# Kernel optimization log

Measured on AMD Instinct MI355X. Metric: run time of the kernel, lower is better.

Reference implementation:

```python
import jax, jax.numpy as jnp
from jax import lax
import numpy as np

H = 48; W = 48; C_IN = 256; A_PER = 3
M = A_PER * H * W            # 6912 anchors
IMG = 768.0                  # square image, clip bound for x and y
OBJ_THR = 0.3; IOU_THR = 0.7; TOP_K = 2000
NEG = -1e9                   # finite sentinel for masked scores


def _make_anchors():
    stride = IMG / H
    base = 2.0 * stride
    ratios = np.array([0.5, 1.0, 2.0])
    ws = base * np.sqrt(ratios)          # [3]
    hs = base / np.sqrt(ratios)
    cx = (np.arange(W) + 0.5) * stride
    cy = (np.arange(H) + 0.5) * stride
    cxg, cyg = np.meshgrid(cx, cy)       # [H, W]
    anc = np.stack([
        cxg[None] - ws[:, None, None] / 2,
        cyg[None] - hs[:, None, None] / 2,
        cxg[None] + ws[:, None, None] / 2,
        cyg[None] + hs[:, None, None] / 2,
    ], axis=-1)                           # [3, H, W, 4] matches (anchor, h, w) flatten order
    return jnp.asarray(anc.reshape(-1, 4), jnp.float32)


def setup_inputs() -> dict:
    key = jax.random.key(0)
    ks = jax.random.split(key, 4)
    x = jax.random.normal(ks[0], (1, C_IN, H, W), jnp.float32)
    conv_w = jax.random.normal(ks[1], (256, 256, 3, 3), jnp.float32) * 0.02
    conv_b = jnp.zeros((256,), jnp.float32)
    det_w = jax.random.normal(ks[2], (3, 256, 1, 1), jnp.float32) * 0.02
    det_b = jnp.zeros((3,), jnp.float32)
    reg_w = jax.random.normal(ks[3], (12, 256, 1, 1), jnp.float32) * 0.02
    reg_b = jnp.zeros((12,), jnp.float32)
    anchors = _make_anchors()
    return {"x": x, "conv_w": conv_w, "conv_b": conv_b, "det_w": det_w,
            "det_b": det_b, "reg_w": reg_w, "reg_b": reg_b, "anchors": anchors}


def reference(x, conv_w, conv_b, det_w, det_b, reg_w, reg_b, anchors):
    # ---- FPN 3x3 conv + RPN head (1x1 convs) ----
    inter = lax.conv_general_dilated(
        x, conv_w, (1, 1), 'SAME',
        dimension_numbers=('NCHW', 'OIHW', 'NCHW')) + conv_b[None, :, None, None]
    obj = jax.nn.sigmoid(jnp.einsum('nchw,oc->nohw', inter, det_w[:, :, 0, 0])
                         + det_b[None, :, None, None])          # [1,3,H,W]
    reg = (jnp.einsum('nchw,oc->nohw', inter, reg_w[:, :, 0, 0])
           + reg_b[None, :, None, None])                        # [1,12,H,W]

    scores = obj.reshape(-1)                                    # [M], (anchor,h,w) order
    deltas = reg.reshape(1, 4, A_PER, H, W).transpose(0, 2, 3, 4, 1).reshape(-1, 4)

    # ---- box decode (preserves the source's cx/cy quirk: cx = y1 + w/2, cy = x1 + h/2) ----
    x1, y1, x2, y2 = anchors[:, 0], anchors[:, 1], anchors[:, 2], anchors[:, 3]
    aw = x2 - x1; ah = y2 - y1
    acx = y1 + aw / 2; acy = x1 + ah / 2
    dx, dy, dw, dh = deltas[:, 0], deltas[:, 1], deltas[:, 2], deltas[:, 3]
    px = acx + dx * aw; py = acy + dy * ah
    pw = aw * jnp.exp(dw); ph = ah * jnp.exp(dh)
    boxes = jnp.stack([px - pw / 2, py - ph / 2, px + pw / 2, py + ph / 2], axis=-1)

    # ---- clip to image ----
    boxes = jnp.clip(boxes, 0.0, IMG)

    # ---- validity: degenerate filter (source's naming quirk) + objectness threshold ----
    hts = boxes[:, 2] - boxes[:, 0]
    wds = boxes[:, 3] - boxes[:, 1]
    valid = (hts > 0) & (wds > 0) & (scores > OBJ_THR)

    # ---- greedy NMS (jit-friendly: sort, pairwise IoU, sequential suppression) ----
    s = jnp.where(valid, scores, NEG)
    order = jnp.argsort(-s)
    b = boxes[order]; v = valid[order]; ss = s[order]
    area = (b[:, 2] - b[:, 0]) * (b[:, 3] - b[:, 1])             # [M]
    iw = jnp.clip(jnp.minimum(b[:, None, 2], b[None, :, 2])
                  - jnp.maximum(b[:, None, 0], b[None, :, 0]), 0.0)
    ih = jnp.clip(jnp.minimum(b[:, None, 3], b[None, :, 3])
                  - jnp.maximum(b[:, None, 1], b[None, :, 1]), 0.0)
    inter_a = iw * ih                                             # [M,M]
    iou = inter_a / jnp.maximum(area[:, None] + area[None, :] - inter_a, 1e-9)

    idx = jnp.arange(M)

    def body(suppressed, i):
        keep_i = v[i] & (~suppressed[i])
        sup = keep_i & (iou[i] > IOU_THR) & (idx > i)
        return suppressed | sup, keep_i

    _, keeps = lax.scan(body, jnp.zeros(M, bool), idx)            # keep mask (sorted order)

    # ---- top-k proposal selection (fixed K, padded with sentinels) ----
    out_s = jnp.where(keeps, ss, NEG)
    topv, topi = lax.top_k(out_s, TOP_K)
    vtop = keeps[topi]
    out_scores = jnp.where(vtop, topv, -1.0)                      # [TOP_K]
    out_boxes = jnp.where(vtop[:, None], b[topi], 0.0)            # [TOP_K, 4]
    return out_scores, out_boxes
```

## Files before the change

kernel.cpp:

```cpp
#include <hip/hip_runtime.h>
#include <cstdint>

#define NPX 2304
#define MM 6912
#define NW 108
#define TOPK 2000
#define NEGV -1000000000.0f
#define OBJ_THRF 0.3f
#define IOU_THRF 0.7f
#define IMGF 768.0f
#define KSPLIT 8

typedef unsigned long long u64;
typedef unsigned int u32;

__device__ __forceinline__ u64 shfl64(u64 v, int src) {
  int lo = __shfl((int)(v & 0xffffffffull), src, 64);
  int hi = __shfl((int)(v >> 32), src, 64);
  return ((u64)(u32)hi << 32) | (u32)lo;
}

__global__ __launch_bounds__(256) void k_wt(const float* __restrict__ cw,
                                            float* __restrict__ wt) {
  __shared__ float t[64][65];
  const int it0 = blockIdx.x * 64;
  const int oc0 = blockIdx.y * 64;
  const int tx = threadIdx.x & 63;
  const int ty = threadIdx.x >> 6;
#pragma unroll
  for (int k = 0; k < 16; ++k) {
    int oc = ty + k * 4;
    t[oc][tx] = cw[(oc0 + oc) * 2304 + it0 + tx];
  }
  __syncthreads();
#pragma unroll
  for (int k = 0; k < 16; ++k) {
    int it = ty + k * 4;
    wt[(it0 + it) * 256 + oc0 + tx] = t[tx][it];
  }
}

__global__ __launch_bounds__(256) void k_conv(const float* __restrict__ x,
                                              const float* __restrict__ wt,
                                              float* __restrict__ part) {
  __shared__ float xs[16 * 8 * 52];
  const int tid = threadIdx.x;
  const int px = blockIdx.x * 256 + tid;
  const int oc0 = blockIdx.y * 16;
  const int ks = blockIdx.z;
  const int row = px / 48, col = px % 48;
  const int r0 = (blockIdx.x * 256) / 48;
  const int rbase = row - r0;

  float acc[16];
#pragma unroll
  for (int k = 0; k < 16; ++k) acc[k] = 0.f;

  for (int icc = 0; icc < 2; ++icc) {
    const int ic0 = ks * 32 + icc * 16;
    for (int e = tid; e < 16 * 8 * 50; e += 256) {
      int ic = e / 400, rem = e % 400;
      int r = rem / 50, c = rem % 50 - 1;
      int gr = r0 - 1 + r;
      float v = 0.f;
      if (c >= 0 && c < 48 && gr >= 0 && gr < 48)
        v = x[(ic0 + ic) * NPX + gr * 48 + c];
      xs[(ic * 8 + r) * 52 + (c + 1)] = v;
    }
    __syncthreads();
    for (int ic = 0; ic < 16; ++ic) {
      float xv[9];
#pragma unroll
      for (int dr = 0; dr < 3; ++dr)
#pragma unroll
        for (int dc = 0; dc < 3; ++dc)
          xv[dr * 3 + dc] = xs[(ic * 8 + rbase + dr) * 52 + col + dc];
      const float* wrow = wt + (size_t)(ic0 + ic) * 9 * 256 + oc0;
#pragma unroll
      for (int t = 0; t < 9; ++t) {
        const float* wp = wrow + t * 256;
#pragma unroll
        for (int k = 0; k < 16; ++k) acc[k] += xv[t] * wp[k];
      }
    }
    __syncthreads();
  }
#pragma unroll
  for (int k = 0; k < 16; ++k)
    part[((size_t)ks * 256 + oc0 + k) * NPX + px] = acc[k];
}

__global__ __launch_bounds__(256) void k_decode(const float* __restrict__ part,
                                                const float* __restrict__ cb,
                                                const float* __restrict__ dw,
                                                const float* __restrict__ db,
                                                const float* __restrict__ rw,
                                                const float* __restrict__ rb,
                                                const float* __restrict__ anch,
                                                float* __restrict__ s,
                                                float4* __restrict__ boxes) {
  __shared__ float wl[256 * 16];
  __shared__ float red[4 * 64 * 17];
  const int tid = threadIdx.x;
  const int pxl = tid & 63;
  const int cq = tid >> 6;
  const int px = blockIdx.x * 64 + pxl;
  for (int e = tid; e < 3840; e += 256) {
    int o = e % 15, c = e / 15;
    wl[c * 16 + o] = (o < 3) ? dw[o * 256 + c] : rw[(o - 3) * 256 + c];
  }
  __syncthreads();
  float acc[15];
#pragma unroll
  for (int o = 0; o < 15; o++) acc[o] = 0.f;
  for (int ci = 0; ci < 64; ++ci) {
    int c = cq * 64 + ci;
    float v = cb[c];
#pragma unroll
    for (int kks = 0; kks < KSPLIT; ++kks)
      v += part[((size_t)kks * 256 + c) * NPX + px];
#pragma unroll
    for (int o = 0; o < 15; o++) acc[o] += v * wl[c * 16 + o];
  }
#pragma unroll
  for (int o = 0; o < 15; o++) red[(cq * 64 + pxl) * 17 + o] = acc[o];
  __syncthreads();
  if (tid < 64) {
    const int p = blockIdx.x * 64 + tid;
    float a[15];
#pragma unroll
    for (int o = 0; o < 15; o++)
      a[o] = red[tid * 17 + o] + red[(64 + tid) * 17 + o] +
             red[(128 + tid) * 17 + o] + red[(192 + tid) * 17 + o];
    const float4* an4 = (const float4*)anch;
#pragma unroll
    for (int aa = 0; aa < 3; ++aa) {
      int m = aa * NPX + p;
      float logit = a[aa] + db[aa];
      float score = 1.f / (1.f + expf(-logit));
      float dxv = a[3 + 0 + aa] + rb[0 + aa];
      float dyv = a[3 + 3 + aa] + rb[3 + aa];
      float dwv = a[3 + 6 + aa] + rb[6 + aa];
      float dhv = a[3 + 9 + aa] + rb[9 + aa];
      float4 an = an4[m];
      float aw = an.z - an.x;
      float ah = an.w - an.y;
      float acx = an.y + aw * 0.5f;
      float acy = an.x + ah * 0.5f;
      float pxc = acx + dxv * aw;
      float pyc = acy + dyv * ah;
      float pw = aw * expf(dwv);
      float ph = ah * expf(dhv);
      float b0 = pxc - pw * 0.5f, b1 = pyc - ph * 0.5f;
      float b2 = pxc + pw * 0.5f, b3 = pyc + ph * 0.5f;
      b0 = fminf(fmaxf(b0, 0.f), IMGF);
      b1 = fminf(fmaxf(b1, 0.f), IMGF);
      b2 = fminf(fmaxf(b2, 0.f), IMGF);
      b3 = fminf(fmaxf(b3, 0.f), IMGF);
      float hts = b2 - b0, wds = b3 - b1;
      bool valid = (hts > 0.f) && (wds > 0.f) && (score > OBJ_THRF);
      s[m] = valid ? score : NEGV;
      boxes[m] = make_float4(b0, b1, b2, b3);
    }
  }
}

__global__ __launch_bounds__(256) void k_sortA(const float* __restrict__ s,
                                               u64* __restrict__ keys) {
  __shared__ u64 lds[1024];
  const int tid = threadIdx.x;
  const int b = blockIdx.x;
  for (int v = tid; v < 1024; v += 256) {
    int i = b * 1024 + v;
    u64 p;
    if (i < MM) {
      u32 u = __float_as_uint(s[i]);
      u = u ^ (u32)(((int)u >> 31) | 0x80000000);
      p = ((u64)(~u) << 32) | (u32)i;
    } else {
      p = ~0ull;
    }
    lds[v] = p;
  }
  for (u32 kk = 2; kk <= 1024; kk <<= 1) {
    for (u32 j = kk >> 1; j > 0; j >>= 1) {
      __syncthreads();
#pragma unroll 2
      for (int t = tid; t < 512; t += 256) {
        int i = ((t & ~(j - 1)) << 1) | (t & (j - 1));
        int l = i | j;
        bool up = ((i & kk) == 0);
        u64 a = lds[i], c = lds[l];
        u64 mn = a < c ? a : c;
        u64 mx = a < c ? c : a;
        lds[i] = up ? mn : mx;
        lds[l] = up ? mx : mn;
      }
    }
  }
  __syncthreads();
  for (int v = tid; v < 1024; v += 256) keys[b * 1024 + v] = lds[v];
}

__global__ __launch_bounds__(256) void k_merge(const u64* __restrict__ in,
                                               u64* __restrict__ outk, int L, int fin,
                                               const float* __restrict__ s,
                                               const float4* __restrict__ boxes,
                                               float* __restrict__ ssc,
                                               float4* __restrict__ sboxes) {
  const int i = blockIdx.x * 256 + threadIdx.x;
  const int pair = i / (2 * L);
  const int r = i - pair * 2 * L;
  const u64* A = in + (size_t)pair * 2 * L;
  const u64* B = A + L;
  int lo = (r > L) ? (r - L) : 0;
  int hi = (r < L) ? r : L;
  while (lo < hi) {
    int mid = (lo + hi) >> 1;
    if (A[mid] < B[r - 1 - mid]) lo = mid + 1; else hi = mid;
  }
  int a = lo, bi = r - lo;
  u64 av = (a < L) ? A[a] : ~0ull;
  u64 bv = (bi < L) ? B[bi] : ~0ull;
  u64 o = (av < bv) ? av : bv;
  outk[i] = o;
  if (fin && i < MM) {
    int idx = (int)(u32)o;
    ssc[i] = s[idx];
    sboxes[i] = boxes[idx];
  }
}

__global__ __launch_bounds__(256) void k_zero(u64* __restrict__ nz) {
  int i = blockIdx.x * 256 + threadIdx.x;
  if (i < MM * 2) nz[i] = 0;
}

__global__ __launch_bounds__(256) void k_mask(const float4* __restrict__ sboxes,
                                              u64* __restrict__ mask_t,
                                              u64* __restrict__ nz) {
  __shared__ float4 rb_[64];
  const int rt = blockIdx.x;
  const int w = blockIdx.y * 4 + (threadIdx.x >> 6);
  const int lane = threadIdx.x & 63;
  if (threadIdx.x < 64) rb_[threadIdx.x] = sboxes[rt * 64 + threadIdx.x];
  __syncthreads();
  if (w < rt) return;
  float4 c = sboxes[w * 64 + lane];
  float areaC = (c.z - c.x) * (c.w - c.y);
  u64 myw = 0;
  for (int r = 0; r < 64; ++r) {
    float4 b = rb_[r];
    float iw = fmaxf(fminf(b.z, c.z) - fmaxf(b.x, c.x), 0.f);
    float ih = fmaxf(fminf(b.w, c.w) - fmaxf(b.y, c.y), 0.f);
    float inter = iw * ih;
    float areaB = (b.z - b.x) * (b.w - b.y);
    float un = fmaxf(areaB + areaC - inter, 1e-9f);
    bool bit = (inter / un) > IOU_THRF;
    u64 bal = __ballot(bit);
    if (lane == r) myw = bal;
  }
  mask_t[(size_t)w * MM + rt * 64 + lane] = myw;
  if (myw) atomicOr(&nz[(rt * 64 + lane) * 2 + (w >> 6)], 1ull << (w & 63));
}

__global__ __launch_bounds__(256) void k_scan(const u64* __restrict__ mask_t,
                                              const u64* __restrict__ nz,
                                              const float* __restrict__ ssc,
                                              const float4* __restrict__ sboxes,
                                              float* __restrict__ out) {
  __shared__ u64 remv[NW];
  __shared__ u64 keepw[NW];
  __shared__ int blist[64];
  __shared__ int nkS;
  __shared__ int kcntS;
  __shared__ int pref[NW];
  const int tid = threadIdx.x;
  if (tid < NW) { remv[tid] = 0; keepw[tid] = 0; }
  if (tid == 0) kcntS = 0;
  __syncthreads();

  for (int c = 0; c < NW; ++c) {
    if (tid < 64) {
      const int lane = tid;
      u64 dg = mask_t[(size_t)c * MM + c * 64 + lane];
      float sv = ssc[c * 64 + lane];
      u64 vb = __ballot(sv > OBJ_THRF);
      u64 w0 = remv[c];
      u64 cand = vb & ~w0;
      u64 above = (lane < 63) ? ~((2ull << lane) - 1ull) : 0ull;
      bool inC = ((cand >> lane) & 1ull) != 0;
      u64 conf = __ballot(inC && ((dg & above & cand) != 0ull));
      u64 kb;
      if (conf == 0ull) {
        kb = cand;
      } else {
        u64 w = w0;
        kb = 0;
        u64 rem = cand;
        while (rem) {
          int b = __ffsll(rem) - 1;
          kb |= (1ull << b);
          w |= shfl64(dg, b);
          rem = vb & ~w;
        }
      }
      int below = __popcll(kb & ((1ull << lane) - 1ull));
      if ((kb >> lane) & 1ull) blist[below] = lane;
      if (lane == 0) {
        keepw[c] = kb;
        nkS = __popcll(kb);
        kcntS += __popcll(kb);
      }
    }
    __syncthreads();
    int nk = nkS;
    if (tid < nk) {
      int row = c * 64 + blist[tid];
      u64 nz0 = nz[row * 2], nz1 = nz[row * 2 + 1];
      if (c < 64) {
        nz0 &= (c < 63) ? ~((2ull << c) - 1ull) : 0ull;
      } else {
        nz0 = 0;
        int cc = c - 64;
        nz1 &= ~((2ull << cc) - 1ull);
      }
      while (nz0) {
        int wv = __ffsll(nz0) - 1; nz0 &= nz0 - 1;
        atomicOr(&remv[wv], mask_t[(size_t)wv * MM + row]);
      }
      while (nz1) {
        int wv = __ffsll(nz1) - 1; nz1 &= nz1 - 1;
        atomicOr(&remv[wv + 64], mask_t[(size_t)(wv + 64) * MM + row]);
      }
    }
    __syncthreads();
    if (kcntS >= TOPK) break;
  }

  if (tid == 0) {
    int run = 0;
    for (int cc = 0; cc < NW; ++cc) { pref[cc] = run; run += __popcll(keepw[cc]); }
  }
  __syncthreads();
  for (int e = tid; e < TOPK * 5; e += 256) out[e] = (e < TOPK) ? -1.0f : 0.0f;
  __syncthreads();
  float4* ob = (float4*)(out + TOPK);
  for (int i = tid; i < MM; i += 256) {
    int cc = i >> 6, b = i & 63;
    u64 kb = keepw[cc];
    if ((kb >> b) & 1ull) {
      int rank = pref[cc] + __popcll(kb & ((1ull << b) - 1ull));
      if (rank < TOPK) {
        out[rank] = ssc[i];
        ob[rank] = sboxes[i];
      }
    }
  }
}

extern "C" void kernel_launch(void* const* d_in, const int* in_sizes, int n_in,
                              void* d_out, int out_size, void* d_ws, size_t ws_size,
                              hipStream_t stream) {
  const float* x  = (const float*)d_in[0];
  const float* cw = (const float*)d_in[1];
  const float* cb = (const float*)d_in[2];
  const float* dw = (const float*)d_in[3];
  const float* db = (const float*)d_in[4];
  const float* rw = (const float*)d_in[5];
  const float* rb = (const float*)d_in[6];
  const float* an = (const float*)d_in[7];
  char* ws = (char*)d_ws;
  float*  part   = (float*)(ws);
  u64*    keysA  = (u64*)(ws);
  u64*    keysB  = (u64*)(ws + 65536);
  u64*    mask   = (u64*)(ws);
  u64*    nz     = (u64*)(ws + 5971968);
  float*  wt     = (float*)(ws + 18874368);
  float*  s      = (float*)(ws + 21233664);
  float4* boxes  = (float4*)(ws + 21261312);
  float*  ssc    = (float*)(ws + 21371904);
  float4* sboxes = (float4*)(ws + 21399552);
  float* out = (float*)d_out;

  hipLaunchKernelGGL(k_wt, dim3(36, 4), dim3(256), 0, stream, cw, wt);
  hipLaunchKernelGGL(k_conv, dim3(9, 16, KSPLIT), dim3(256), 0, stream, x, wt, part);
  hipLaunchKernelGGL(k_decode, dim3(36), dim3(256), 0, stream, part, cb, dw, db, rw, rb, an, s, boxes);
  hipLaunchKernelGGL(k_zero, dim3(54), dim3(256), 0, stream, nz);
  hipLaunchKernelGGL(k_sortA, dim3(8), dim3(256), 0, stream, s, keysA);
  hipLaunchKernelGGL(k_merge, dim3(32), dim3(256), 0, stream, keysA, keysB, 1024, 0, s, boxes, ssc, sboxes);
  hipLaunchKernelGGL(k_merge, dim3(32), dim3(256), 0, stream, keysB, keysA, 2048, 0, s, boxes, ssc, sboxes);
  hipLaunchKernelGGL(k_merge, dim3(32), dim3(256), 0, stream, keysA, keysB, 4096, 1, s, boxes, ssc, sboxes);
  hipLaunchKernelGGL(k_mask, dim3(108, 27), dim3(256), 0, stream, sboxes, mask, nz);
  hipLaunchKernelGGL(k_scan, dim3(1), dim3(256), 0, stream, mask, nz, ssc, sboxes, out);
}
```

Measured before the change: 267.2 us.

## Halve conv output-channel tile and split decode into parallel partial and finish kernels

The conv kernel now computes 8 output channels per block instead of 16, with smaller input-channel chunks, which doubles the grid to raise occupancy and parallelism. The decode stage is split into k_dq, which spreads the channel quarters across 144 small blocks and writes partial sums to workspace, and k_dfin, which reduces those sums and decodes boxes. This replaces the single 36-block decode that leaned on shared memory. The cost is one extra kernel launch, an extra global round trip for the partials, and more reloading of the halo input per conv block.

```diff
diff --git a/kernel.cpp b/kernel.cpp
--- a/kernel.cpp
+++ b/kernel.cpp
@@ -43,22 +43,22 @@
 __global__ __launch_bounds__(256) void k_conv(const float* __restrict__ x,
                                               const float* __restrict__ wt,
                                               float* __restrict__ part) {
-  __shared__ float xs[16 * 8 * 52];
+  __shared__ float xs[8 * 8 * 52];
   const int tid = threadIdx.x;
   const int px = blockIdx.x * 256 + tid;
-  const int oc0 = blockIdx.y * 16;
+  const int oc0 = blockIdx.y * 8;
   const int ks = blockIdx.z;
   const int row = px / 48, col = px % 48;
   const int r0 = (blockIdx.x * 256) / 48;
   const int rbase = row - r0;
 
-  float acc[16];
-#pragma unroll
-  for (int k = 0; k < 16; ++k) acc[k] = 0.f;
-
-  for (int icc = 0; icc < 2; ++icc) {
-    const int ic0 = ks * 32 + icc * 16;
-    for (int e = tid; e < 16 * 8 * 50; e += 256) {
+  float acc[8];
+#pragma unroll
+  for (int k = 0; k < 8; ++k) acc[k] = 0.f;
+
+  for (int icc = 0; icc < 4; ++icc) {
+    const int ic0 = ks * 32 + icc * 8;
+    for (int e = tid; e < 8 * 8 * 50; e += 256) {
       int ic = e / 400, rem = e % 400;
       int r = rem / 50, c = rem % 50 - 1;
       int gr = r0 - 1 + r;
@@ -68,7 +68,7 @@
       xs[(ic * 8 + r) * 52 + (c + 1)] = v;
     }
     __syncthreads();
-    for (int ic = 0; ic < 16; ++ic) {
+    for (int ic = 0; ic < 8; ++ic) {
       float xv[9];
 #pragma unroll
       for (int dr = 0; dr < 3; ++dr)
@@ -80,39 +80,35 @@
       for (int t = 0; t < 9; ++t) {
         const float* wp = wrow + t * 256;
 #pragma unroll
-        for (int k = 0; k < 16; ++k) acc[k] += xv[t] * wp[k];
+        for (int k = 0; k < 8; ++k) acc[k] += xv[t] * wp[k];
       }
     }
     __syncthreads();
   }
 #pragma unroll
-  for (int k = 0; k < 16; ++k)
+  for (int k = 0; k < 8; ++k)
     part[((size_t)ks * 256 + oc0 + k) * NPX + px] = acc[k];
 }
 
-__global__ __launch_bounds__(256) void k_decode(const float* __restrict__ part,
-                                                const float* __restrict__ cb,
-                                                const float* __restrict__ dw,
-                                                const float* __restrict__ db,
-                                                const float* __restrict__ rw,
-                                                const float* __restrict__ rb,
-                                                const float* __restrict__ anch,
-                                                float* __restrict__ s,
-                                                float4* __restrict__ boxes) {
-  __shared__ float wl[256 * 16];
-  __shared__ float red[4 * 64 * 17];
+__global__ __launch_bounds__(64) void k_dq(const float* __restrict__ part,
+                                           const float* __restrict__ cb,
+                                           const float* __restrict__ dw,
+                                           const float* __restrict__ rw,
+                                           float* __restrict__ qacc) {
+  __shared__ float wl[64 * 16];
   const int tid = threadIdx.x;
-  const int pxl = tid & 63;
-  const int cq = tid >> 6;
-  const int px = blockIdx.x * 64 + pxl;
-  for (int e = tid; e < 3840; e += 256) {
-    int o = e % 15, c = e / 15;
-    wl[c * 16 + o] = (o < 3) ? dw[o * 256 + c] : rw[(o - 3) * 256 + c];
+  const int cq = blockIdx.y;
+  const int px = blockIdx.x * 64 + tid;
+  for (int e = tid; e < 960; e += 64) {
+    int o = e % 15, ci = e / 15;
+    int c = cq * 64 + ci;
+    wl[ci * 16 + o] = (o < 3) ? dw[o * 256 + c] : rw[(o - 3) * 256 + c];
   }
   __syncthreads();
   float acc[15];
 #pragma unroll
   for (int o = 0; o < 15; o++) acc[o] = 0.f;
+#pragma unroll 4
   for (int ci = 0; ci < 64; ++ci) {
     int c = cq * 64 + ci;
     float v = cb[c];
@@ -120,48 +116,57 @@
     for (int kks = 0; kks < KSPLIT; ++kks)
       v += part[((size_t)kks * 256 + c) * NPX + px];
 #pragma unroll
-    for (int o = 0; o < 15; o++) acc[o] += v * wl[c * 16 + o];
-  }
-#pragma unroll
-  for (int o = 0; o < 15; o++) red[(cq * 64 + pxl) * 17 + o] = acc[o];
-  __syncthreads();
-  if (tid < 64) {
-    const int p = blockIdx.x * 64 + tid;
-    float a[15];
-#pragma unroll
-    for (int o = 0; o < 15; o++)
-      a[o] = red[tid * 17 + o] + red[(64 + tid) * 17 + o] +
-             red[(128 + tid) * 17 + o] + red[(192 + tid) * 17 + o];
-    const float4* an4 = (const float4*)anch;
-#pragma unroll
-    for (int aa = 0; aa < 3; ++aa) {
-      int m = aa * NPX + p;
-      float logit = a[aa] + db[aa];
-      float score = 1.f / (1.f + expf(-logit));
-      float dxv = a[3 + 0 + aa] + rb[0 + aa];
-      float dyv = a[3 + 3 + aa] + rb[3 + aa];
-      float dwv = a[3 + 6 + aa] + rb[6 + aa];
-      float dhv = a[3 + 9 + aa] + rb[9 + aa];
-      float4 an = an4[m];
-      float aw = an.z - an.x;
-      float ah = an.w - an.y;
-      float acx = an.y + aw * 0.5f;
-      float acy = an.x + ah * 0.5f;
-      float pxc = acx + dxv * aw;
-      float pyc = acy + dyv * ah;
-      float pw = aw * expf(dwv);
-      float ph = ah * expf(dhv);
-      float b0 = pxc - pw * 0.5f, b1 = pyc - ph * 0.5f;
-      float b2 = pxc + pw * 0.5f, b3 = pyc + ph * 0.5f;
-      b0 = fminf(fmaxf(b0, 0.f), IMGF);
-      b1 = fminf(fmaxf(b1, 0.f), IMGF);
-      b2 = fminf(fmaxf(b2, 0.f), IMGF);
-      b3 = fminf(fmaxf(b3, 0.f), IMGF);
-      float hts = b2 - b0, wds = b3 - b1;
-      bool valid = (hts > 0.f) && (wds > 0.f) && (score > OBJ_THRF);
-      s[m] = valid ? score : NEGV;
-      boxes[m] = make_float4(b0, b1, b2, b3);
-    }
+    for (int o = 0; o < 15; o++) acc[o] += v * wl[ci * 16 + o];
+  }
+#pragma unroll
+  for (int o = 0; o < 15; o++)
+    qacc[((size_t)cq * NPX + px) * 16 + o] = acc[o];
+}
+
+__global__ __launch_bounds__(64) void k_dfin(const float* __restrict__ qacc,
+                                             const float* __restrict__ db,
+                                             const float* __restrict__ rb,
+                                             const float* __restrict__ anch,
+                                             float* __restrict__ s,
+                                             float4* __restrict__ boxes) {
+  const int tid = threadIdx.x;
+  const int p = blockIdx.x * 64 + tid;
+  float a[15];
+#pragma unroll
+  for (int o = 0; o < 15; o++)
+    a[o] = qacc[((size_t)0 * NPX + p) * 16 + o] +
+           qacc[((size_t)1 * NPX + p) * 16 + o] +
+           qacc[((size_t)2 * NPX + p) * 16 + o] +
+           qacc[((size_t)3 * NPX + p) * 16 + o];
+  const float4* an4 = (const float4*)anch;
+#pragma unroll
+  for (int aa = 0; aa < 3; ++aa) {
+    int m = aa * NPX + p;
+    float logit = a[aa] + db[aa];
+    float score = 1.f / (1.f + expf(-logit));
+    float dxv = a[3 + 0 + aa] + rb[0 + aa];
+    float dyv = a[3 + 3 + aa] + rb[3 + aa];
+    float dwv = a[3 + 6 + aa] + rb[6 + aa];
+    float dhv = a[3 + 9 + aa] + rb[9 + aa];
+    float4 an = an4[m];
+    float aw = an.z - an.x;
+    float ah = an.w - an.y;
+    float acx = an.y + aw * 0.5f;
+    float acy = an.x + ah * 0.5f;
+    float pxc = acx + dxv * aw;
+    float pyc = acy + dyv * ah;
+    float pw = aw * expf(dwv);
+    float ph = ah * expf(dhv);
+    float b0 = pxc - pw * 0.5f, b1 = pyc - ph * 0.5f;
+    float b2 = pxc + pw * 0.5f, b3 = pyc + ph * 0.5f;
+    b0 = fminf(fmaxf(b0, 0.f), IMGF);
+    b1 = fminf(fmaxf(b1, 0.f), IMGF);
+    b2 = fminf(fmaxf(b2, 0.f), IMGF);
+    b3 = fminf(fmaxf(b3, 0.f), IMGF);
+    float hts = b2 - b0, wds = b3 - b1;
+    bool valid = (hts > 0.f) && (wds > 0.f) && (score > OBJ_THRF);
+    s[m] = valid ? score : NEGV;
+    boxes[m] = make_float4(b0, b1, b2, b3);
   }
 }
 
@@ -377,6 +382,7 @@
   u64*    mask   = (u64*)(ws);
   u64*    nz     = (u64*)(ws + 5971968);
   float*  wt     = (float*)(ws + 18874368);
+  float*  qacc   = (float*)(ws + 18874368);
   float*  s      = (float*)(ws + 21233664);
   float4* boxes  = (float4*)(ws + 21261312);
   float*  ssc    = (float*)(ws + 21371904);
@@ -384,8 +390,9 @@
   float* out = (float*)d_out;
 
   hipLaunchKernelGGL(k_wt, dim3(36, 4), dim3(256), 0, stream, cw, wt);
-  hipLaunchKernelGGL(k_conv, dim3(9, 16, KSPLIT), dim3(256), 0, stream, x, wt, part);
-  hipLaunchKernelGGL(k_decode, dim3(36), dim3(256), 0, stream, part, cb, dw, db, rw, rb, an, s, boxes);
+  hipLaunchKernelGGL(k_conv, dim3(9, 32, KSPLIT), dim3(256), 0, stream, x, wt, part);
+  hipLaunchKernelGGL(k_dq, dim3(36, 4), dim3(64), 0, stream, part, cb, dw, rw, qacc);
+  hipLaunchKernelGGL(k_dfin, dim3(36), dim3(64), 0, stream, qacc, db, rb, an, s, boxes);
   hipLaunchKernelGGL(k_zero, dim3(54), dim3(256), 0, stream, nz);
   hipLaunchKernelGGL(k_sortA, dim3(8), dim3(256), 0, stream, s, keysA);
   hipLaunchKernelGGL(k_merge, dim3(32), dim3(256), 0, stream, keysA, keysB, 1024, 0, s, boxes, ssc, sboxes);
```

Result: slower. 282.6 us (+5.8%).

## Fuse merge passes into one LDS kernel, fold nz zeroing, preload scan data

Applied to the files above, without the earlier changes.

Replaces three global-memory merge-pass launches with one 1024-thread block that runs all merge passes in shared memory, and folds the nz zeroing into the sort kernel, removing four launches. The serial scan kernel now preloads the diagonal mask words and sorted scores into LDS, so the per-chunk loop no longer waits on global loads. The cost is that the merges run on a single CU, and the scan kernel uses more shared memory (about 83 KB), which limits it to one block.

```diff
diff --git a/kernel.cpp b/kernel.cpp
--- a/kernel.cpp
+++ b/kernel.cpp
@@ -166,10 +166,12 @@
 }
 
 __global__ __launch_bounds__(256) void k_sortA(const float* __restrict__ s,
-                                               u64* __restrict__ keys) {
+                                               u64* __restrict__ keys,
+                                               u64* __restrict__ nz) {
   __shared__ u64 lds[1024];
   const int tid = threadIdx.x;
   const int b = blockIdx.x;
+  for (int i = b * 256 + tid; i < MM * 2; i += 8 * 256) nz[i] = 0;
   for (int v = tid; v < 1024; v += 256) {
     int i = b * 1024 + v;
     u64 p;
@@ -202,38 +204,45 @@
   for (int v = tid; v < 1024; v += 256) keys[b * 1024 + v] = lds[v];
 }
 
-__global__ __launch_bounds__(256) void k_merge(const u64* __restrict__ in,
-                                               u64* __restrict__ outk, int L, int fin,
-                                               const float* __restrict__ s,
-                                               const float4* __restrict__ boxes,
-                                               float* __restrict__ ssc,
-                                               float4* __restrict__ sboxes) {
-  const int i = blockIdx.x * 256 + threadIdx.x;
-  const int pair = i / (2 * L);
-  const int r = i - pair * 2 * L;
-  const u64* A = in + (size_t)pair * 2 * L;
-  const u64* B = A + L;
-  int lo = (r > L) ? (r - L) : 0;
-  int hi = (r < L) ? r : L;
-  while (lo < hi) {
-    int mid = (lo + hi) >> 1;
-    if (A[mid] < B[r - 1 - mid]) lo = mid + 1; else hi = mid;
-  }
-  int a = lo, bi = r - lo;
-  u64 av = (a < L) ? A[a] : ~0ull;
-  u64 bv = (bi < L) ? B[bi] : ~0ull;
-  u64 o = (av < bv) ? av : bv;
-  outk[i] = o;
-  if (fin && i < MM) {
-    int idx = (int)(u32)o;
+__global__ __launch_bounds__(1024) void k_mtail(const u64* __restrict__ keysA,
+                                                const float* __restrict__ s,
+                                                const float4* __restrict__ boxes,
+                                                float* __restrict__ ssc,
+                                                float4* __restrict__ sboxes) {
+  __shared__ u64 A[8192];
+  __shared__ u64 B[8192];
+  const int tid = threadIdx.x;
+  for (int v = tid; v < 8192; v += 1024) A[v] = keysA[v];
+  __syncthreads();
+
+  const u64* in = A;
+  u64* out = B;
+#pragma unroll 1
+  for (int L = 1024; L <= 4096; L <<= 1) {
+    for (int i = tid; i < 8192; i += 1024) {
+      int pair = i / (2 * L);
+      int r = i - pair * 2 * L;
+      const u64* Ap = in + pair * 2 * L;
+      const u64* Bp = Ap + L;
+      int lo = (r > L) ? (r - L) : 0;
+      int hi = (r < L) ? r : L;
+      while (lo < hi) {
+        int mid = (lo + hi) >> 1;
+        if (Ap[mid] < Bp[r - 1 - mid]) lo = mid + 1; else hi = mid;
+      }
+      int a = lo, bi = r - lo;
+      u64 av = (a < L) ? Ap[a] : ~0ull;
+      u64 bv = (bi < L) ? Bp[bi] : ~0ull;
+      out[i] = (av < bv) ? av : bv;
+    }
+    __syncthreads();
+    const u64* t = in; in = out; out = (u64*)t;
+  }
+  for (int i = tid; i < MM; i += 1024) {
+    int idx = (int)(u32)in[i];
     ssc[i] = s[idx];
     sboxes[i] = boxes[idx];
   }
-}
-
-__global__ __launch_bounds__(256) void k_zero(u64* __restrict__ nz) {
-  int i = blockIdx.x * 256 + threadIdx.x;
-  if (i < MM * 2) nz[i] = 0;
 }
 
 __global__ __launch_bounds__(256) void k_mask(const float4* __restrict__ sboxes,
@@ -269,6 +278,8 @@
                                               const float* __restrict__ ssc,
                                               const float4* __restrict__ sboxes,
                                               float* __restrict__ out) {
+  __shared__ u64 diagL[NW * 64];
+  __shared__ float sscL[MM];
   __shared__ u64 remv[NW];
   __shared__ u64 keepw[NW];
   __shared__ int blist[64];
@@ -276,6 +287,9 @@
   __shared__ int kcntS;
   __shared__ int pref[NW];
   const int tid = threadIdx.x;
+  for (int e = tid; e < NW * 64; e += 256)
+    diagL[e] = mask_t[(size_t)(e >> 6) * MM + (e >> 6) * 64 + (e & 63)];
+  for (int e = tid; e < MM; e += 256) sscL[e] = ssc[e];
   if (tid < NW) { remv[tid] = 0; keepw[tid] = 0; }
   if (tid == 0) kcntS = 0;
   __syncthreads();
@@ -283,8 +297,8 @@
   for (int c = 0; c < NW; ++c) {
     if (tid < 64) {
       const int lane = tid;
-      u64 dg = mask_t[(size_t)c * MM + c * 64 + lane];
-      float sv = ssc[c * 64 + lane];
+      u64 dg = diagL[c * 64 + lane];
+      float sv = sscL[c * 64 + lane];
       u64 vb = __ballot(sv > OBJ_THRF);
       u64 w0 = remv[c];
       u64 cand = vb & ~w0;
@@ -352,7 +366,7 @@
     if ((kb >> b) & 1ull) {
       int rank = pref[cc] + __popcll(kb & ((1ull << b) - 1ull));
       if (rank < TOPK) {
-        out[rank] = ssc[i];
+        out[rank] = sscL[i];
         ob[rank] = sboxes[i];
       }
     }
@@ -373,7 +387,6 @@
   char* ws = (char*)d_ws;
   float*  part   = (float*)(ws);
   u64*    keysA  = (u64*)(ws);
-  u64*    keysB  = (u64*)(ws + 65536);
   u64*    mask   = (u64*)(ws);
   u64*    nz     = (u64*)(ws + 5971968);
   float*  wt     = (float*)(ws + 18874368);
@@ -386,11 +399,8 @@
   hipLaunchKernelGGL(k_wt, dim3(36, 4), dim3(256), 0, stream, cw, wt);
   hipLaunchKernelGGL(k_conv, dim3(9, 16, KSPLIT), dim3(256), 0, stream, x, wt, part);
   hipLaunchKernelGGL(k_decode, dim3(36), dim3(256), 0, stream, part, cb, dw, db, rw, rb, an, s, boxes);
-  hipLaunchKernelGGL(k_zero, dim3(54), dim3(256), 0, stream, nz);
-  hipLaunchKernelGGL(k_sortA, dim3(8), dim3(256), 0, stream, s, keysA);
-  hipLaunchKernelGGL(k_merge, dim3(32), dim3(256), 0, stream, keysA, keysB, 1024, 0, s, boxes, ssc, sboxes);
-  hipLaunchKernelGGL(k_merge, dim3(32), dim3(256), 0, stream, keysB, keysA, 2048, 0, s, boxes, ssc, sboxes);
-  hipLaunchKernelGGL(k_merge, dim3(32), dim3(256), 0, stream, keysA, keysB, 4096, 1, s, boxes, ssc, sboxes);
+  hipLaunchKernelGGL(k_sortA, dim3(8), dim3(256), 0, stream, s, keysA, nz);
+  hipLaunchKernelGGL(k_mtail, dim3(1), dim3(1024), 0, stream, keysA, s, boxes, ssc, sboxes);
   hipLaunchKernelGGL(k_mask, dim3(108, 27), dim3(256), 0, stream, sboxes, mask, nz);
   hipLaunchKernelGGL(k_scan, dim3(1), dim3(256), 0, stream, mask, nz, ssc, sboxes, out);
 }
```

Result: slower. 292.8 us (+9.6%).

## Parallelize NMS suppression updates and stage diagonal masks in LDS

Applied to the files above, without the earlier changes.

The single-block NMS scan now preloads all diagonal mask words and sorted scores into shared memory, and prefetches each chunk's nonzero-word bitmap into LDS. The per-kept-box serial loop over suppression words becomes a prefix-scanned list of (word, row) pairs processed by all 256 threads. This reduces load imbalance and global latency on the serial critical path. The zeroing kernel is folded into the sort kernel to save a launch. The cost is extra shared memory (about 83 KB) and additional barriers per chunk.

```diff
diff --git a/kernel.cpp b/kernel.cpp
--- a/kernel.cpp
+++ b/kernel.cpp
@@ -13,6 +13,7 @@
 
 typedef unsigned long long u64;
 typedef unsigned int u32;
+typedef unsigned short u16;
 
 __device__ __forceinline__ u64 shfl64(u64 v, int src) {
   int lo = __shfl((int)(v & 0xffffffffull), src, 64);
@@ -166,10 +167,12 @@
 }
 
 __global__ __launch_bounds__(256) void k_sortA(const float* __restrict__ s,
-                                               u64* __restrict__ keys) {
+                                               u64* __restrict__ keys,
+                                               u64* __restrict__ nz) {
   __shared__ u64 lds[1024];
   const int tid = threadIdx.x;
   const int b = blockIdx.x;
+  for (int i = b * 256 + tid; i < MM * 2; i += 8 * 256) nz[i] = 0;
   for (int v = tid; v < 1024; v += 256) {
     int i = b * 1024 + v;
     u64 p;
@@ -231,11 +234,6 @@
   }
 }
 
-__global__ __launch_bounds__(256) void k_zero(u64* __restrict__ nz) {
-  int i = blockIdx.x * 256 + threadIdx.x;
-  if (i < MM * 2) nz[i] = 0;
-}
-
 __global__ __launch_bounds__(256) void k_mask(const float4* __restrict__ sboxes,
                                               u64* __restrict__ mask_t,
                                               u64* __restrict__ nz) {
@@ -269,22 +267,31 @@
                                               const float* __restrict__ ssc,
                                               const float4* __restrict__ sboxes,
                                               float* __restrict__ out) {
+  __shared__ u64 diagL[NW * 64];
+  __shared__ float sscL[MM];
+  __shared__ u16 pairs[MM];
+  __shared__ u64 nzTmp[128];
   __shared__ u64 remv[NW];
   __shared__ u64 keepw[NW];
   __shared__ int blist[64];
   __shared__ int nkS;
   __shared__ int kcntS;
+  __shared__ int TS;
   __shared__ int pref[NW];
   const int tid = threadIdx.x;
+  for (int e = tid; e < NW * 64; e += 256)
+    diagL[e] = mask_t[(size_t)(e >> 6) * MM + (e >> 6) * 64 + (e & 63)];
+  for (int e = tid; e < MM; e += 256) sscL[e] = ssc[e];
   if (tid < NW) { remv[tid] = 0; keepw[tid] = 0; }
   if (tid == 0) kcntS = 0;
   __syncthreads();
 
   for (int c = 0; c < NW; ++c) {
+    if (tid >= 128) nzTmp[tid - 128] = nz[c * 128 + (tid - 128)];
     if (tid < 64) {
       const int lane = tid;
-      u64 dg = mask_t[(size_t)c * MM + c * 64 + lane];
-      float sv = ssc[c * 64 + lane];
+      u64 dg = diagL[c * 64 + lane];
+      float sv = sscL[c * 64 + lane];
       u64 vb = __ballot(sv > OBJ_THRF);
       u64 w0 = remv[c];
       u64 cand = vb & ~w0;
@@ -314,25 +321,47 @@
       }
     }
     __syncthreads();
-    int nk = nkS;
-    if (tid < nk) {
-      int row = c * 64 + blist[tid];
-      u64 nz0 = nz[row * 2], nz1 = nz[row * 2 + 1];
-      if (c < 64) {
-        nz0 &= (c < 63) ? ~((2ull << c) - 1ull) : 0ull;
-      } else {
-        nz0 = 0;
-        int cc = c - 64;
-        nz1 &= ~((2ull << cc) - 1ull);
-      }
-      while (nz0) {
-        int wv = __ffsll(nz0) - 1; nz0 &= nz0 - 1;
-        atomicOr(&remv[wv], mask_t[(size_t)wv * MM + row]);
-      }
-      while (nz1) {
-        int wv = __ffsll(nz1) - 1; nz1 &= nz1 - 1;
-        atomicOr(&remv[wv + 64], mask_t[(size_t)(wv + 64) * MM + row]);
-      }
+    const int nk = nkS;
+    if (tid < 64) {
+      u64 n0 = 0, n1 = 0;
+      int b = 0;
+      if (tid < nk) {
+        b = blist[tid];
+        n0 = nzTmp[2 * b];
+        n1 = nzTmp[2 * b + 1];
+        if (c < 64) {
+          n0 &= (c < 63) ? ~((2ull << c) - 1ull) : 0ull;
+        } else {
+          n0 = 0;
+          n1 &= ~((2ull << (c - 64)) - 1ull);
+        }
+      }
+      int cnt = __popcll(n0) + __popcll(n1);
+      int sc = cnt;
+#pragma unroll
+      for (int d = 1; d < 64; d <<= 1) {
+        int o = __shfl_up(sc, d, 64);
+        if (tid >= d) sc += o;
+      }
+      int base = sc - cnt;
+      if (tid == 63) TS = sc;
+      int k = 0;
+      while (n0) {
+        int wv = __ffsll(n0) - 1; n0 &= n0 - 1;
+        pairs[base + k] = (u16)((wv << 6) | b); ++k;
+      }
+      while (n1) {
+        int wv = __ffsll(n1) - 1; n1 &= n1 - 1;
+        pairs[base + k] = (u16)(((wv + 64) << 6) | b); ++k;
+      }
+    }
+    __syncthreads();
+    const int T = TS;
+    for (int p = tid; p < T; p += 256) {
+      u32 pr = pairs[p];
+      int wv = pr >> 6, b = pr & 63;
+      u64 v = mask_t[(size_t)wv * MM + c * 64 + b];
+      atomicOr(&remv[wv], v);
     }
     __syncthreads();
     if (kcntS >= TOPK) break;
@@ -352,7 +381,7 @@
     if ((kb >> b) & 1ull) {
       int rank = pref[cc] + __popcll(kb & ((1ull << b) - 1ull));
       if (rank < TOPK) {
-        out[rank] = ssc[i];
+        out[rank] = sscL[i];
         ob[rank] = sboxes[i];
       }
     }
@@ -386,8 +415,7 @@
   hipLaunchKernelGGL(k_wt, dim3(36, 4), dim3(256), 0, stream, cw, wt);
   hipLaunchKernelGGL(k_conv, dim3(9, 16, KSPLIT), dim3(256), 0, stream, x, wt, part);
   hipLaunchKernelGGL(k_decode, dim3(36), dim3(256), 0, stream, part, cb, dw, db, rw, rb, an, s, boxes);
-  hipLaunchKernelGGL(k_zero, dim3(54), dim3(256), 0, stream, nz);
-  hipLaunchKernelGGL(k_sortA, dim3(8), dim3(256), 0, stream, s, keysA);
+  hipLaunchKernelGGL(k_sortA, dim3(8), dim3(256), 0, stream, s, keysA, nz);
   hipLaunchKernelGGL(k_merge, dim3(32), dim3(256), 0, stream, keysA, keysB, 1024, 0, s, boxes, ssc, sboxes);
   hipLaunchKernelGGL(k_merge, dim3(32), dim3(256), 0, stream, keysB, keysA, 2048, 0, s, boxes, ssc, sboxes);
   hipLaunchKernelGGL(k_merge, dim3(32), dim3(256), 0, stream, keysA, keysB, 4096, 1, s, boxes, ssc, sboxes);
```

Measured after the change: 270.1 us. No clear change (+1.1%).
